# Performance work log

Hardware: AMD Instinct MI355X
Metric: run time of the kernel (lower is better)

Reference implementation:

```python
import jax, jax.numpy as jnp
import numpy as np

N = 50000       # nodes
E = 800000      # edges
F_IN = 197      # node_feature_dim
H = 256         # hidden_dim
HEADS = 8
HD = H // HEADS # 32
L = 5           # num_layers
FF = 4 * H      # 1024
C = 2           # num_classes
ED = 2          # edge_feature_dim
SCALE = float(np.sqrt(HD))


def _ln(x, g, b):
    m = x.mean(-1, keepdims=True)
    v = ((x - m) ** 2).mean(-1, keepdims=True)
    return (x - m) / jnp.sqrt(v + 1e-5) * g + b


def setup_inputs() -> dict:
    key = jax.random.key(0)
    ks = iter(jax.random.split(key, 40))
    d = {}
    d["x"] = jax.random.normal(next(ks), (N, F_IN), dtype=jnp.float32)
    d["edge_index"] = jax.random.randint(next(ks), (2, E), 0, N, dtype=jnp.int64)
    d["edge_attr"] = jax.random.normal(next(ks), (E, ED), dtype=jnp.float32)
    xav = lambda k, sh: jax.random.normal(k, sh, dtype=jnp.float32) * float(np.sqrt(2.0 / (sh[-2] + sh[-1])))
    # input projection + LN
    d["in_W"] = xav(next(ks), (F_IN, H)); d["in_b"] = jnp.zeros((H,), jnp.float32)
    d["in_g"] = jnp.ones((H,), jnp.float32); d["in_bb"] = jnp.zeros((H,), jnp.float32)
    # stacked per-layer params (leading dim L)
    d["Wq"] = xav(next(ks), (L, H, H)); d["Wk"] = xav(next(ks), (L, H, H)); d["Wv"] = xav(next(ks), (L, H, H))
    d["We"] = xav(next(ks), (L, ED, HEADS)); d["be"] = jnp.zeros((L, HEADS), jnp.float32)
    d["Wo"] = xav(next(ks), (L, H, H)); d["bo"] = jnp.zeros((L, H), jnp.float32)
    d["ln1_g"] = jnp.ones((L, H), jnp.float32); d["ln1_b"] = jnp.zeros((L, H), jnp.float32)
    d["ln2_g"] = jnp.ones((L, H), jnp.float32); d["ln2_b"] = jnp.zeros((L, H), jnp.float32)
    d["f1_W"] = xav(next(ks), (L, H, FF)); d["f1_b"] = jnp.zeros((L, FF), jnp.float32)
    d["f2_W"] = xav(next(ks), (L, FF, H)); d["f2_b"] = jnp.zeros((L, H), jnp.float32)
    # classifier
    d["cls1_W"] = xav(next(ks), (H, H // 2)); d["cls1_b"] = jnp.zeros((H // 2,), jnp.float32)
    d["cls2_W"] = xav(next(ks), (H // 2, C)); d["cls2_b"] = jnp.zeros((C,), jnp.float32)
    return d


def _forward(x, edge_index, edge_attr, in_W, in_b, in_g, in_bb,
             Wq, Wk, Wv, We, be, Wo, bo, ln1_g, ln1_b, ln2_g, ln2_b,
             f1_W, f1_b, f2_W, f2_b, cls1_W, cls1_b, cls2_W, cls2_b):
    src, dst = edge_index[0], edge_index[1]  # message flows src -> dst
    h = jax.nn.gelu(_ln(x @ in_W + in_b, in_g, in_bb), approximate=False)

    def layer(h, p):
        wq, wk, wv, we, b_e, wo, b_o, g1, b1, g2, b2, w1, bf1, w2, bf2 = p
        hn = _ln(h, g1, b1)
        q = (hn @ wq).reshape(-1, HEADS, HD)
        k = (hn @ wk).reshape(-1, HEADS, HD)
        v = (hn @ wv).reshape(-1, HEADS, HD)
        edge_bias = edge_attr @ we + b_e                        # (E, HEADS)
        score = (q[dst] * k[src]).sum(-1) / SCALE + edge_bias   # (E, HEADS)
        # segment softmax over destination nodes
        mx = jax.ops.segment_max(score, dst, num_segments=N)
        mx = jnp.where(jnp.isfinite(mx), mx, 0.0)
        ex = jnp.exp(score - mx[dst])
        denom = jax.ops.segment_sum(ex, dst, num_segments=N)
        w = ex / (denom[dst] + 1e-16)                           # (E, HEADS)
        msg = w[:, :, None] * v[src]                            # (E, HEADS, HD)
        agg = jax.ops.segment_sum(msg.reshape(-1, H), dst, num_segments=N)
        out = agg @ wo + b_o
        out = _ln(out + h, g2, b2)                              # residual_proj = Identity
        ffn = jax.nn.gelu(out @ w1 + bf1, approximate=False) @ w2 + bf2
        return out + ffn, None

    params = (Wq, Wk, Wv, We, be, Wo, bo, ln1_g, ln1_b, ln2_g, ln2_b, f1_W, f1_b, f2_W, f2_b)
    h, _ = jax.lax.scan(layer, h, params)
    logits = jax.nn.gelu(h @ cls1_W + cls1_b, approximate=False) @ cls2_W + cls2_b
    probs = jax.nn.softmax(logits, axis=-1)
    return logits, probs


def reference(x, edge_index, edge_attr, in_W, in_b, in_g, in_bb,
              Wq, Wk, Wv, We, be, Wo, bo, ln1_g, ln1_b, ln2_g, ln2_b,
              f1_W, f1_b, f2_W, f2_b, cls1_W, cls1_b, cls2_W, cls2_b):
    return _forward(x, edge_index, edge_attr, in_W, in_b, in_g, in_bb,
                    Wq, Wk, Wv, We, be, Wo, bo, ln1_g, ln1_b, ln2_g, ln2_b,
                    f1_W, f1_b, f2_W, f2_b, cls1_W, cls1_b, cls2_W, cls2_b)
```

## Files before the change

### kernel.cpp

```cpp
#include <hip/hip_runtime.h>
#include <math.h>

#define NN 50000
#define NE 800000
#define FIN 197
#define KIN 224
#define H 256
#define HEADS 8
#define HD 32
#define LAYERS 5
#define FF 1024
#define INV_SCALE 0.17677669529663687f

typedef __attribute__((ext_vector_type(8))) short short8;
typedef __attribute__((ext_vector_type(4))) float f32x4;
typedef unsigned short ushort;

__device__ __forceinline__ float gelu_f(float x) {
    float x2 = x * x;
    float u = __builtin_fmaf(0.044715f * x2, x, x);
    float e = __builtin_amdgcn_exp2f(-2.3022075f * u);
    return x * __builtin_amdgcn_rcpf(1.0f + e);
}
__device__ __forceinline__ ushort f2b(float f) {
    unsigned u = __float_as_uint(f);
    u += 0x7fffu + ((u >> 16) & 1u);
    return (ushort)(u >> 16);
}
__device__ __forceinline__ float b2f(ushort b) {
    return __uint_as_float(((unsigned)b) << 16);
}
__device__ __forceinline__ float dot2b(unsigned a, unsigned b) {
    float a0 = __uint_as_float(a << 16), a1 = __uint_as_float(a & 0xffff0000u);
    float b0 = __uint_as_float(b << 16), b1 = __uint_as_float(b & 0xffff0000u);
    return a0 * b0 + a1 * b1;
}

__device__ __forceinline__ void load16_lds(const ushort* gp, ushort* lp) {
    __builtin_amdgcn_global_load_lds(
        (const __attribute__((address_space(1))) unsigned int*)gp,
        (__attribute__((address_space(3))) unsigned int*)lp,
        16, 0, 0);
}

__global__ __launch_bounds__(256) void gemm_bf16_kernel(
    const ushort* __restrict__ A, int lda,
    const ushort* __restrict__ Bt,
    const float* __restrict__ bias,
    const float* __restrict__ res, int ldr,
    float* __restrict__ Cf, ushort* __restrict__ Cb, int ldc,
    int n, int K, int act, int gx)
{
    __shared__ ushort As[2][128 * 32];
    __shared__ ushort Bs[2][64 * 32];
    int tid = threadIdx.x;
    int lane = tid & 63;
    int wave = tid >> 6;

    int tiles_y = (n + 127) >> 7;
    int lin = blockIdx.x;
    int gsz = gx * 8;
    int group = lin / gsz;
    int rem = lin - group * gsz;
    int rows_left = tiles_y - group * 8;
    int rg = rows_left < 8 ? rows_left : 8;
    int r = rem % rg;
    int c = rem / rg;
    int brow = (group * 8 + r) * 128;
    int bcol = c * 64;

    f32x4 acc[2][4] = {};
    int m0 = lane & 15;
    int rdc = ((lane >> 4) ^ ((lane >> 1) & 3)) * 8;

    int rA = lane >> 2;
    int c8s = (((lane & 3) ^ ((lane >> 3) & 3)) * 8);

    long arow0, arow1, brow0;
    {
        int gr0 = brow + wave * 32 + rA;        if (gr0 >= n) gr0 = n - 1;
        int gr1 = brow + wave * 32 + 16 + rA;   if (gr1 >= n) gr1 = n - 1;
        arow0 = (long)gr0 * lda;
        arow1 = (long)gr1 * lda;
        brow0 = (long)(bcol + wave * 16 + rA) * K;
    }
    int loA0 = (wave * 32) * 32;
    int loA1 = (wave * 32 + 16) * 32;
    int loB  = (wave * 16) * 32;

    int nt = K >> 5;
    load16_lds(A + arow0 + c8s, &As[0][loA0]);
    load16_lds(A + arow1 + c8s, &As[0][loA1]);
    load16_lds(Bt + brow0 + c8s, &Bs[0][loB]);
    __syncthreads();

    for (int t = 0; t < nt; ++t) {
        int p = t & 1;
        if (t + 1 < nt) {
            int k0 = (t + 1) << 5;
            load16_lds(A + arow0 + k0 + c8s, &As[p ^ 1][loA0]);
            load16_lds(A + arow1 + k0 + c8s, &As[p ^ 1][loA1]);
            load16_lds(Bt + brow0 + k0 + c8s, &Bs[p ^ 1][loB]);
        }
        short8 af[2], bfr[4];
        #pragma unroll
        for (int i = 0; i < 2; ++i)
            af[i] = *(const short8*)&As[p][(wave * 32 + i * 16 + m0) * 32 + rdc];
        #pragma unroll
        for (int j = 0; j < 4; ++j)
            bfr[j] = *(const short8*)&Bs[p][(j * 16 + m0) * 32 + rdc];
        #pragma unroll
        for (int i = 0; i < 2; ++i)
            #pragma unroll
            for (int j = 0; j < 4; ++j)
                acc[i][j] = __builtin_amdgcn_mfma_f32_16x16x32_bf16(af[i], bfr[j], acc[i][j], 0, 0, 0);
        __syncthreads();
    }

    int crow0 = (lane >> 4) * 4;
    int ccol = lane & 15;
    #pragma unroll
    for (int i = 0; i < 2; ++i) {
        #pragma unroll
        for (int rr = 0; rr < 4; ++rr) {
            int grow = brow + wave * 32 + i * 16 + crow0 + rr;
            if (grow >= n) continue;
            #pragma unroll
            for (int j = 0; j < 4; ++j) {
                int gcol = bcol + j * 16 + ccol;
                float v = acc[i][j][rr];
                if (bias) v += bias[gcol];
                if (act) v = gelu_f(v);
                if (res) v += res[(long)grow * ldr + gcol];
                if (Cf) Cf[(long)grow * ldc + gcol] = v;
                if (Cb) Cb[(long)grow * ldc + gcol] = f2b(v);
            }
        }
    }
}

__global__ __launch_bounds__(256) void ln256_kernel(
    const float* __restrict__ af, const ushort* __restrict__ ab,
    const float* __restrict__ res,
    const float* __restrict__ g, const float* __restrict__ bta,
    float* __restrict__ outf, ushort* __restrict__ outb, int n, int post_gelu)
{
    int row = blockIdx.x * 4 + (threadIdx.x >> 6);
    if (row >= n) return;
    int lane = threadIdx.x & 63;
    float4 v;
    if (af) {
        v = *(const float4*)(af + (long)row * H + lane * 4);
    } else {
        ushort4 vb = *(const ushort4*)(ab + (long)row * H + lane * 4);
        v.x = b2f(vb.x); v.y = b2f(vb.y); v.z = b2f(vb.z); v.w = b2f(vb.w);
    }
    if (res) {
        float4 r = *(const float4*)(res + (long)row * H + lane * 4);
        v.x += r.x; v.y += r.y; v.z += r.z; v.w += r.w;
    }
    float s = v.x + v.y + v.z + v.w;
    #pragma unroll
    for (int off = 1; off < 64; off <<= 1) s += __shfl_xor(s, off);
    float mean = s * (1.0f / H);
    float dx = v.x - mean, dy = v.y - mean, dz = v.z - mean, dw = v.w - mean;
    float qs = dx * dx + dy * dy + dz * dz + dw * dw;
    #pragma unroll
    for (int off = 1; off < 64; off <<= 1) qs += __shfl_xor(qs, off);
    float rstd = rsqrtf(qs * (1.0f / H) + 1e-5f);
    float4 gg = *(const float4*)(g + lane * 4);
    float4 bb = *(const float4*)(bta + lane * 4);
    float4 o;
    o.x = dx * rstd * gg.x + bb.x;
    o.y = dy * rstd * gg.y + bb.y;
    o.z = dz * rstd * gg.z + bb.z;
    o.w = dw * rstd * gg.w + bb.w;
    if (post_gelu) { o.x = gelu_f(o.x); o.y = gelu_f(o.y); o.z = gelu_f(o.z); o.w = gelu_f(o.w); }
    if (outf) *(float4*)(outf + (long)row * H + lane * 4) = o;
    if (outb) {
        ushort4 ob = { f2b(o.x), f2b(o.y), f2b(o.z), f2b(o.w) };
        *(ushort4*)(outb + (long)row * H + lane * 4) = ob;
    }
}

__global__ __launch_bounds__(256) void xcast_kernel(const float* __restrict__ x,
                                                    ushort* __restrict__ xb)
{
    long i = (long)blockIdx.x * 256 + threadIdx.x;
    if (i >= (long)NN * KIN) return;
    int n = (int)(i / KIN), c = (int)(i % KIN);
    xb[i] = (c < FIN) ? f2b(x[(long)n * FIN + c]) : (ushort)0;
}

__global__ __launch_bounds__(256) void wtin_kernel(const float* __restrict__ W,
                                                   ushort* __restrict__ Wt)
{
    int i = blockIdx.x * 256 + threadIdx.x;
    if (i >= 256 * KIN) return;
    int m = i / KIN, k = i % KIN;
    Wt[i] = (k < FIN) ? f2b(W[(long)k * H + m]) : (ushort)0;
}

__global__ __launch_bounds__(256) void wtqkv_kernel(
    const float* __restrict__ Wq, const float* __restrict__ Wk,
    const float* __restrict__ Wv, ushort* __restrict__ out)
{
    long i = (long)blockIdx.x * 256 + threadIdx.x;
    if (i >= (long)LAYERS * 768 * 256) return;
    int l = (int)(i / (768 * 256));
    int r = (int)(i % (768 * 256));
    int m = r >> 8, k = r & 255;
    const float* W = (m < 256) ? Wq : ((m < 512) ? Wk : Wv);
    out[i] = f2b(W[(long)l * 65536 + (long)k * 256 + (m & 255)]);
}

__global__ __launch_bounds__(256) void wtgen_kernel(
    const float* __restrict__ W, ushort* __restrict__ out, int L, int K, int M)
{
    long i = (long)blockIdx.x * 256 + threadIdx.x;
    if (i >= (long)L * K * M) return;
    int l = (int)(i / ((long)K * M));
    int r = (int)(i % ((long)K * M));
    int m = r / K, k = r % K;
    out[i] = f2b(W[(long)l * K * M + (long)k * M + m]);
}

__global__ __launch_bounds__(256) void deg_kernel(const int* __restrict__ dst,
                                                   int* __restrict__ deg)
{
    int e = blockIdx.x * 256 + threadIdx.x;
    if (e >= NE) return;
    atomicAdd(&deg[dst[e]], 1);
}

__global__ __launch_bounds__(256) void scan1_kernel(const int* __restrict__ deg,
                                                     int* __restrict__ rowptr,
                                                     int* __restrict__ bsum)
{
    __shared__ int buf[256];
    int tid = threadIdx.x;
    int i = blockIdx.x * 256 + tid;
    int v = (i < NN) ? deg[i] : 0;
    buf[tid] = v;
    __syncthreads();
    #pragma unroll
    for (int off = 1; off < 256; off <<= 1) {
        int t = (tid >= off) ? buf[tid - off] : 0;
        __syncthreads();
        buf[tid] += t;
        __syncthreads();
    }
    if (i < NN) rowptr[i] = buf[tid] - v;
    if (tid == 255) bsum[blockIdx.x] = buf[255];
}

__global__ __launch_bounds__(256) void scan2_kernel(int* __restrict__ bsum, int nb)
{
    __shared__ int buf[256];
    int tid = threadIdx.x;
    int v = (tid < nb) ? bsum[tid] : 0;
    buf[tid] = v;
    __syncthreads();
    #pragma unroll
    for (int off = 1; off < 256; off <<= 1) {
        int t = (tid >= off) ? buf[tid - off] : 0;
        __syncthreads();
        buf[tid] += t;
        __syncthreads();
    }
    if (tid < nb) bsum[tid] = buf[tid] - v;
}

__global__ __launch_bounds__(256) void scan3_kernel(int* __restrict__ rowptr,
                                                     const int* __restrict__ bsum)
{
    int i = blockIdx.x * 256 + threadIdx.x;
    if (i < NN) rowptr[i] += bsum[blockIdx.x];
    if (i == 0) rowptr[NN] = NE;
}

__global__ __launch_bounds__(256) void fill_kernel(
    const int* __restrict__ src, const int* __restrict__ dst,
    const float* __restrict__ ea, const int* __restrict__ rowptr,
    int* __restrict__ cursor, int* __restrict__ csr_src,
    float2* __restrict__ csr_ea)
{
    int e = blockIdx.x * 256 + threadIdx.x;
    if (e >= NE) return;
    int d = dst[e];
    int pos = atomicAdd(&cursor[d], 1);
    int j = rowptr[d] + pos;
    csr_src[j] = src[e];
    csr_ea[j] = *(const float2*)(ea + 2 * e);
}

__global__ __launch_bounds__(256) void attn_kernel(
    const ushort* __restrict__ qkv,
    const int* __restrict__ rowptr, const int* __restrict__ csr_src,
    const float2* __restrict__ csr_ea,
    const float* __restrict__ We, const float* __restrict__ be,
    ushort* __restrict__ aggb)
{
    int node = blockIdx.x * 4 + (threadIdx.x >> 6);
    if (node >= NN) return;
    int lane = threadIdx.x & 63;
    int h = lane >> 3;
    const float L2E = 1.4426950408889634f;
    float w0 = We[h] * L2E, w1 = We[8 + h] * L2E, bb = be[h] * L2E;
    const float c1 = INV_SCALE * L2E;

    uint2 q2 = *(const uint2*)(qkv + (long)node * 768 + lane * 4);
    int jbeg = rowptr[node], jend = rowptr[node + 1];

    float m = -1e30f, l = 0.f;
    float a0 = 0.f, a1 = 0.f, a2 = 0.f, a3 = 0.f;

    uint2 kA = {0, 0}, vA = {0, 0}, kB = {0, 0}, vB = {0, 0};
    float2 eaA = {0.f, 0.f}, eaB = {0.f, 0.f};

    if (jbeg < jend) {
        int s = csr_src[jbeg]; eaA = csr_ea[jbeg];
        const ushort* kr = qkv + (long)s * 768 + 256;
        kA = *(const uint2*)(kr + lane * 4);
        vA = *(const uint2*)(kr + 256 + lane * 4);
    }
    if (jbeg + 1 < jend) {
        int s = csr_src[jbeg + 1]; eaB = csr_ea[jbeg + 1];
        const ushort* kr = qkv + (long)s * 768 + 256;
        kB = *(const uint2*)(kr + lane * 4);
        vB = *(const uint2*)(kr + 256 + lane * 4);
    }

    int j = jbeg;
    for (; j + 1 < jend; j += 2) {
        uint2 k1 = kA, v1 = vA, k2 = kB, v2 = vB;
        float2 e1 = eaA, e2 = eaB;
        if (j + 2 < jend) {
            int s = csr_src[j + 2]; eaA = csr_ea[j + 2];
            const ushort* kr = qkv + (long)s * 768 + 256;
            kA = *(const uint2*)(kr + lane * 4);
            vA = *(const uint2*)(kr + 256 + lane * 4);
        }
        if (j + 3 < jend) {
            int s = csr_src[j + 3]; eaB = csr_ea[j + 3];
            const ushort* kr = qkv + (long)s * 768 + 256;
            kB = *(const uint2*)(kr + lane * 4);
            vB = *(const uint2*)(kr + 256 + lane * 4);
        }
        float p1 = dot2b(q2.x, k1.x) + dot2b(q2.y, k1.y);
        float p2 = dot2b(q2.x, k2.x) + dot2b(q2.y, k2.y);
        p1 += __shfl_xor(p1, 1);  p2 += __shfl_xor(p2, 1);
        p1 += __shfl_xor(p1, 2);  p2 += __shfl_xor(p2, 2);
        p1 += __shfl_xor(p1, 4);  p2 += __shfl_xor(p2, 4);
        float s1 = p1 * c1 + e1.x * w0 + e1.y * w1 + bb;
        float s2 = p2 * c1 + e2.x * w0 + e2.y * w1 + bb;
        float mp = fmaxf(s1, s2);
        float x1 = __builtin_amdgcn_exp2f(s1 - mp);
        float x2 = __builtin_amdgcn_exp2f(s2 - mp);
        float lp = x1 + x2;
        float b0 = x1 * __uint_as_float(v1.x << 16)          + x2 * __uint_as_float(v2.x << 16);
        float b1 = x1 * __uint_as_float(v1.x & 0xffff0000u)  + x2 * __uint_as_float(v2.x & 0xffff0000u);
        float b2 = x1 * __uint_as_float(v1.y << 16)          + x2 * __uint_as_float(v2.y << 16);
        float b3 = x1 * __uint_as_float(v1.y & 0xffff0000u)  + x2 * __uint_as_float(v2.y & 0xffff0000u);
        float mn = fmaxf(m, mp);
        float so = __builtin_amdgcn_exp2f(m - mn);
        float sp = __builtin_amdgcn_exp2f(mp - mn);
        l  = l  * so + lp * sp;
        a0 = a0 * so + b0 * sp;
        a1 = a1 * so + b1 * sp;
        a2 = a2 * so + b2 * sp;
        a3 = a3 * so + b3 * sp;
        m = mn;
    }
    if (j < jend) {
        float p1 = dot2b(q2.x, kA.x) + dot2b(q2.y, kA.y);
        p1 += __shfl_xor(p1, 1);
        p1 += __shfl_xor(p1, 2);
        p1 += __shfl_xor(p1, 4);
        float s1 = p1 * c1 + eaA.x * w0 + eaA.y * w1 + bb;
        float mn = fmaxf(m, s1);
        float so = __builtin_amdgcn_exp2f(m - mn);
        float e  = __builtin_amdgcn_exp2f(s1 - mn);
        l  = l  * so + e;
        a0 = a0 * so + e * __uint_as_float(vA.x << 16);
        a1 = a1 * so + e * __uint_as_float(vA.x & 0xffff0000u);
        a2 = a2 * so + e * __uint_as_float(vA.y << 16);
        a3 = a3 * so + e * __uint_as_float(vA.y & 0xffff0000u);
    }
    float inv = 1.0f / (l + 1e-16f);
    ushort4 o = { f2b(a0 * inv), f2b(a1 * inv), f2b(a2 * inv), f2b(a3 * inv) };
    *(ushort4*)(aggb + (long)node * 256 + lane * 4) = o;
}

__global__ __launch_bounds__(256) void cls_kernel(
    const float* __restrict__ t1, const float* __restrict__ W,
    const float* __restrict__ b, float* __restrict__ out)
{
    int i = blockIdx.x * 256 + threadIdx.x;
    if (i >= NN) return;
    const float* tp = t1 + (long)i * 128;
    float a0 = 0.f, a1 = 0.f;
    #pragma unroll
    for (int j = 0; j < 128; j += 4) {
        float4 t = *(const float4*)(tp + j);
        a0 += t.x * W[(j + 0) * 2] + t.y * W[(j + 1) * 2] + t.z * W[(j + 2) * 2] + t.w * W[(j + 3) * 2];
        a1 += t.x * W[(j + 0) * 2 + 1] + t.y * W[(j + 1) * 2 + 1] + t.z * W[(j + 2) * 2 + 1] + t.w * W[(j + 3) * 2 + 1];
    }
    float l0 = a0 + b[0], l1 = a1 + b[1];
    out[(long)i * 2 + 0] = l0;
    out[(long)i * 2 + 1] = l1;
    float mx = fmaxf(l0, l1);
    float p0 = expf(l0 - mx), p1 = expf(l1 - mx);
    float sden = p0 + p1;
    out[2L * NN + (long)i * 2 + 0] = p0 / sden;
    out[2L * NN + (long)i * 2 + 1] = p1 / sden;
}

extern "C" void kernel_launch(void* const* d_in, const int* in_sizes, int n_in,
                              void* d_out, int out_size, void* d_ws, size_t ws_size,
                              hipStream_t stream) {
    const float* x      = (const float*)d_in[0];
    const int*   ei     = (const int*)d_in[1];
    const float* ea     = (const float*)d_in[2];
    const float* in_W   = (const float*)d_in[3];
    const float* in_b   = (const float*)d_in[4];
    const float* in_g   = (const float*)d_in[5];
    const float* in_bb  = (const float*)d_in[6];
    const float* Wq     = (const float*)d_in[7];
    const float* Wk     = (const float*)d_in[8];
    const float* Wv     = (const float*)d_in[9];
    const float* We     = (const float*)d_in[10];
    const float* be     = (const float*)d_in[11];
    const float* Wo     = (const float*)d_in[12];
    const float* bo     = (const float*)d_in[13];
    const float* ln1_g  = (const float*)d_in[14];
    const float* ln1_b  = (const float*)d_in[15];
    const float* ln2_g  = (const float*)d_in[16];
    const float* ln2_b  = (const float*)d_in[17];
    const float* f1_W   = (const float*)d_in[18];
    const float* f1_b   = (const float*)d_in[19];
    const float* f2_W   = (const float*)d_in[20];
    const float* f2_b   = (const float*)d_in[21];
    const float* cls1_W = (const float*)d_in[22];
    const float* cls1_b = (const float*)d_in[23];
    const float* cls2_W = (const float*)d_in[24];
    const float* cls2_b = (const float*)d_in[25];
    float* out = (float*)d_out;

    const int* src = ei;
    const int* dst = ei + NE;

    char* w = (char*)d_ws;
    float* B0 = (float*)w;            w += (size_t)NN * H * 4;
    ushort* hb = (ushort*)w;          w += (size_t)NN * H * 2;
    char* pool = w;                   w += (size_t)NN * 1024 * 2;
    ushort* qkv  = (ushort*)pool;
    ushort* aggb = (ushort*)(pool + (size_t)NN * 768 * 2);
    float*  tproj = (float*)pool;
    ushort* xb   = (ushort*)(pool + (size_t)NN * H * 4);
    ushort* tb   = (ushort*)pool;
    float*  t1   = (float*)pool;
    int* deg    = (int*)w;            w += (size_t)NN * 4;
    int* cursor = (int*)w;            w += (size_t)NN * 4;
    int* rowptr = (int*)w;            w += (size_t)(NN + 2) * 4;
    int* bsum   = (int*)w;            w += 1024;
    int* csr_src = (int*)w;           w += (size_t)NE * 4;
    float2* csr_ea = (float2*)w;      w += (size_t)NE * 8;
    ushort* wqkv_t = (ushort*)w;      w += (size_t)LAYERS * 768 * 256 * 2;
    ushort* wo_t  = (ushort*)w;       w += (size_t)LAYERS * 65536 * 2;
    ushort* f1_t  = (ushort*)w;       w += (size_t)LAYERS * 262144 * 2;
    ushort* f2_t  = (ushort*)w;       w += (size_t)LAYERS * 262144 * 2;
    ushort* c1_t  = (ushort*)w;       w += (size_t)32768 * 2;
    ushort* inw_t = (ushort*)w;       w += (size_t)256 * KIN * 2;

    dim3 blk(256);
    const int ln_grid = (NN + 3) / 4;
    const int e_grid = (NE + 255) / 256;
    const int n_grid = (NN + 255) / 256;
    const int ty = (NN + 127) / 128;

    hipMemsetAsync(deg, 0, (size_t)NN * 4, stream);
    hipMemsetAsync(cursor, 0, (size_t)NN * 4, stream);
    deg_kernel<<<e_grid, blk, 0, stream>>>(dst, deg);
    scan1_kernel<<<n_grid, blk, 0, stream>>>(deg, rowptr, bsum);
    scan2_kernel<<<1, blk, 0, stream>>>(bsum, n_grid);
    scan3_kernel<<<n_grid, blk, 0, stream>>>(rowptr, bsum);
    fill_kernel<<<e_grid, blk, 0, stream>>>(src, dst, ea, rowptr, cursor, csr_src, csr_ea);

    wtqkv_kernel<<<(int)(((long)LAYERS * 768 * 256 + 255) / 256), blk, 0, stream>>>(Wq, Wk, Wv, wqkv_t);
    wtgen_kernel<<<(int)(((long)LAYERS * 65536 + 255) / 256), blk, 0, stream>>>(Wo, wo_t, LAYERS, 256, 256);
    wtgen_kernel<<<(int)(((long)LAYERS * 262144 + 255) / 256), blk, 0, stream>>>(f1_W, f1_t, LAYERS, 256, 1024);
    wtgen_kernel<<<(int)(((long)LAYERS * 262144 + 255) / 256), blk, 0, stream>>>(f2_W, f2_t, LAYERS, 1024, 256);
    wtgen_kernel<<<(32768 + 255) / 256, blk, 0, stream>>>(cls1_W, c1_t, 1, 256, 128);
    wtin_kernel<<<(256 * KIN + 255) / 256, blk, 0, stream>>>(in_W, inw_t);

    xcast_kernel<<<(int)(((long)NN * KIN + 255) / 256), blk, 0, stream>>>(x, xb);
    {
        gemm_bf16_kernel<<<4 * ty, blk, 0, stream>>>(xb, KIN, inw_t, in_b, nullptr, 0,
                                                     tproj, nullptr, H, NN, KIN, 0, 4);
        ln256_kernel<<<ln_grid, blk, 0, stream>>>(tproj, nullptr, nullptr, in_g, in_bb, B0, nullptr, NN, 1);
    }

    for (int l = 0; l < LAYERS; ++l) {
        const float* we  = We + (long)l * 16;
        const float* bel = be + (long)l * 8;
        const float* bol = bo + (long)l * H;
        const float* g1 = ln1_g + (long)l * H;
        const float* b1 = ln1_b + (long)l * H;
        const float* g2 = ln2_g + (long)l * H;
        const float* b2 = ln2_b + (long)l * H;
        const float* bf1 = f1_b + (long)l * FF;
        const float* bf2 = f2_b + (long)l * H;

        ln256_kernel<<<ln_grid, blk, 0, stream>>>(B0, nullptr, nullptr, g1, b1, nullptr, hb, NN, 0);

        gemm_bf16_kernel<<<12 * ty, blk, 0, stream>>>(hb, H, wqkv_t + (long)l * 768 * 256,
            nullptr, nullptr, 0, nullptr, qkv, 768, NN, H, 0, 12);
        attn_kernel<<<(NN + 3) / 4, blk, 0, stream>>>(qkv, rowptr, csr_src, csr_ea, we, bel, aggb);

        gemm_bf16_kernel<<<4 * ty, blk, 0, stream>>>(aggb, H, wo_t + (long)l * 65536,
            bol, nullptr, 0, nullptr, qkv, H, NN, H, 0, 4);
        ln256_kernel<<<ln_grid, blk, 0, stream>>>(nullptr, qkv, B0, g2, b2, B0, hb, NN, 0);

        gemm_bf16_kernel<<<16 * ty, blk, 0, stream>>>(hb, H, f1_t + (long)l * 262144,
            bf1, nullptr, 0, nullptr, tb, FF, NN, H, 1, 16);
        gemm_bf16_kernel<<<4 * ty, blk, 0, stream>>>(tb, FF, f2_t + (long)l * 262144,
            bf2, B0, H, B0, (l == LAYERS - 1) ? hb : nullptr, H, NN, FF, 0, 4);
    }

    {
        gemm_bf16_kernel<<<2 * ty, blk, 0, stream>>>(hb, H, c1_t, cls1_b, nullptr, 0,
                                                     t1, nullptr, 128, NN, H, 1, 2);
        cls_kernel<<<n_grid, blk, 0, stream>>>(t1, cls2_W, cls2_b, out);
    }
}
```

Before: 2.385 ms.

## Sort attention nodes by degree and deepen edge prefetch to four

Adds a counting sort of nodes by in-degree (histogram, bin scan, scatter) so the attention kernel processes high-degree nodes first and places nodes of similar degree in the same block. This targets load imbalance and tail effects from variable-degree rows. The attention loop now keeps four edges of K/V in flight instead of two, to hide more gather latency, at the cost of more registers. Node order loses locality in the query and output writes.

```diff
diff --git a/kernel.cpp b/kernel.cpp
--- a/kernel.cpp
+++ b/kernel.cpp
@@ -294,15 +294,105 @@
     csr_ea[j] = *(const float2*)(ea + 2 * e);
 }
 
+__global__ __launch_bounds__(256) void hist_kernel(const int* __restrict__ rowptr,
+                                                   int* __restrict__ bins)
+{
+    int i = blockIdx.x * 256 + threadIdx.x;
+    if (i >= NN) return;
+    int d = rowptr[i + 1] - rowptr[i];
+    int b = d > 255 ? 0 : 255 - d;
+    atomicAdd(&bins[b], 1);
+}
+
+__global__ __launch_bounds__(256) void binscan_kernel(const int* __restrict__ bins,
+                                                      int* __restrict__ binoff)
+{
+    __shared__ int buf[256];
+    int tid = threadIdx.x;
+    int v = bins[tid];
+    buf[tid] = v;
+    __syncthreads();
+    #pragma unroll
+    for (int off = 1; off < 256; off <<= 1) {
+        int t = (tid >= off) ? buf[tid - off] : 0;
+        __syncthreads();
+        buf[tid] += t;
+        __syncthreads();
+    }
+    binoff[tid] = buf[tid] - v;
+}
+
+__global__ __launch_bounds__(256) void order_kernel(const int* __restrict__ rowptr,
+                                                    int* __restrict__ binoff,
+                                                    int* __restrict__ order)
+{
+    int i = blockIdx.x * 256 + threadIdx.x;
+    if (i >= NN) return;
+    int d = rowptr[i + 1] - rowptr[i];
+    int b = d > 255 ? 0 : 255 - d;
+    int pos = atomicAdd(&binoff[b], 1);
+    order[pos] = i;
+}
+
+#define LOADE(idx, kbuf, vbuf, ebuf)                                   \
+    { int s_ = csr_src[idx]; ebuf = csr_ea[idx];                       \
+      const ushort* kr_ = qkv + (long)s_ * 768 + 256;                  \
+      kbuf = *(const uint2*)(kr_ + lane * 4);                          \
+      vbuf = *(const uint2*)(kr_ + 256 + lane * 4); }
+
+#define PAIR(k1, v1, e1, k2, v2, e2)                                               \
+    { float p1 = dot2b(q2.x, (k1).x) + dot2b(q2.y, (k1).y);                        \
+      float p2 = dot2b(q2.x, (k2).x) + dot2b(q2.y, (k2).y);                        \
+      p1 += __shfl_xor(p1, 1);  p2 += __shfl_xor(p2, 1);                           \
+      p1 += __shfl_xor(p1, 2);  p2 += __shfl_xor(p2, 2);                           \
+      p1 += __shfl_xor(p1, 4);  p2 += __shfl_xor(p2, 4);                           \
+      float s1 = p1 * c1 + (e1).x * w0 + (e1).y * w1 + bb;                         \
+      float s2 = p2 * c1 + (e2).x * w0 + (e2).y * w1 + bb;                         \
+      float mp = fmaxf(s1, s2);                                                    \
+      float x1 = __builtin_amdgcn_exp2f(s1 - mp);                                  \
+      float x2 = __builtin_amdgcn_exp2f(s2 - mp);                                  \
+      float lp = x1 + x2;                                                          \
+      float b0 = x1 * __uint_as_float((v1).x << 16)         + x2 * __uint_as_float((v2).x << 16);          \
+      float b1 = x1 * __uint_as_float((v1).x & 0xffff0000u) + x2 * __uint_as_float((v2).x & 0xffff0000u);  \
+      float b2 = x1 * __uint_as_float((v1).y << 16)         + x2 * __uint_as_float((v2).y << 16);          \
+      float b3 = x1 * __uint_as_float((v1).y & 0xffff0000u) + x2 * __uint_as_float((v2).y & 0xffff0000u);  \
+      float mn = fmaxf(m, mp);                                                     \
+      float so = __builtin_amdgcn_exp2f(m - mn);                                   \
+      float sp = __builtin_amdgcn_exp2f(mp - mn);                                  \
+      l  = l  * so + lp * sp;                                                      \
+      a0 = a0 * so + b0 * sp;                                                      \
+      a1 = a1 * so + b1 * sp;                                                      \
+      a2 = a2 * so + b2 * sp;                                                      \
+      a3 = a3 * so + b3 * sp;                                                      \
+      m = mn; }
+
+#define SINGLE(kb, vb, eb)                                                         \
+    { float p1 = dot2b(q2.x, (kb).x) + dot2b(q2.y, (kb).y);                        \
+      p1 += __shfl_xor(p1, 1);                                                     \
+      p1 += __shfl_xor(p1, 2);                                                     \
+      p1 += __shfl_xor(p1, 4);                                                     \
+      float s1 = p1 * c1 + (eb).x * w0 + (eb).y * w1 + bb;                         \
+      float mn = fmaxf(m, s1);                                                     \
+      float so = __builtin_amdgcn_exp2f(m - mn);                                   \
+      float e_ = __builtin_amdgcn_exp2f(s1 - mn);                                  \
+      l  = l  * so + e_;                                                           \
+      a0 = a0 * so + e_ * __uint_as_float((vb).x << 16);                           \
+      a1 = a1 * so + e_ * __uint_as_float((vb).x & 0xffff0000u);                   \
+      a2 = a2 * so + e_ * __uint_as_float((vb).y << 16);                           \
+      a3 = a3 * so + e_ * __uint_as_float((vb).y & 0xffff0000u);                   \
+      m = mn; }
+
 __global__ __launch_bounds__(256) void attn_kernel(
     const ushort* __restrict__ qkv,
     const int* __restrict__ rowptr, const int* __restrict__ csr_src,
     const float2* __restrict__ csr_ea,
     const float* __restrict__ We, const float* __restrict__ be,
+    const int* __restrict__ order,
     ushort* __restrict__ aggb)
 {
-    int node = blockIdx.x * 4 + (threadIdx.x >> 6);
-    if (node >= NN) return;
+    int widx = blockIdx.x * 4 + (threadIdx.x >> 6);
+    if (widx >= NN) return;
+    int node = order[widx];
     int lane = threadIdx.x & 63;
     int h = lane >> 3;
     const float L2E = 1.4426950408889634f;
@@ -315,78 +405,29 @@
     float m = -1e30f, l = 0.f;
     float a0 = 0.f, a1 = 0.f, a2 = 0.f, a3 = 0.f;
 
-    uint2 kA = {0, 0}, vA = {0, 0}, kB = {0, 0}, vB = {0, 0};
-    float2 eaA = {0.f, 0.f}, eaB = {0.f, 0.f};
-
-    if (jbeg < jend) {
-        int s = csr_src[jbeg]; eaA = csr_ea[jbeg];
-        const ushort* kr = qkv + (long)s * 768 + 256;
-        kA = *(const uint2*)(kr + lane * 4);
-        vA = *(const uint2*)(kr + 256 + lane * 4);
-    }
-    if (jbeg + 1 < jend) {
-        int s = csr_src[jbeg + 1]; eaB = csr_ea[jbeg + 1];
-        const ushort* kr = qkv + (long)s * 768 + 256;
-        kB = *(const uint2*)(kr + lane * 4);
-        vB = *(const uint2*)(kr + 256 + lane * 4);
-    }
+    uint2 k0v = {0,0}, v0v = {0,0}, k1v = {0,0}, v1v = {0,0};
+    uint2 k2v = {0,0}, v2v = {0,0}, k3v = {0,0}, v3v = {0,0};
+    float2 e0v = {0.f,0.f}, e1v = {0.f,0.f}, e2v = {0.f,0.f}, e3v = {0.f,0.f};
+
+    if (jbeg + 0 < jend) LOADE(jbeg + 0, k0v, v0v, e0v);
+    if (jbeg + 1 < jend) LOADE(jbeg + 1, k1v, v1v, e1v);
+    if (jbeg + 2 < jend) LOADE(jbeg + 2, k2v, v2v, e2v);
+    if (jbeg + 3 < jend) LOADE(jbeg + 3, k3v, v3v, e3v);
 
     int j = jbeg;
-    for (; j + 1 < jend; j += 2) {
-        uint2 k1 = kA, v1 = vA, k2 = kB, v2 = vB;
-        float2 e1 = eaA, e2 = eaB;
-        if (j + 2 < jend) {
-            int s = csr_src[j + 2]; eaA = csr_ea[j + 2];
-            const ushort* kr = qkv + (long)s * 768 + 256;
-            kA = *(const uint2*)(kr + lane * 4);
-            vA = *(const uint2*)(kr + 256 + lane * 4);
-        }
-        if (j + 3 < jend) {
-            int s = csr_src[j + 3]; eaB = csr_ea[j + 3];
-            const ushort* kr = qkv + (long)s * 768 + 256;
-            kB = *(const uint2*)(kr + lane * 4);
-            vB = *(const uint2*)(kr + 256 + lane * 4);
-        }
-        float p1 = dot2b(q2.x, k1.x) + dot2b(q2.y, k1.y);
-        float p2 = dot2b(q2.x, k2.x) + dot2b(q2.y, k2.y);
-        p1 += __shfl_xor(p1, 1);  p2 += __shfl_xor(p2, 1);
-        p1 += __shfl_xor(p1, 2);  p2 += __shfl_xor(p2, 2);
-        p1 += __shfl_xor(p1, 4);  p2 += __shfl_xor(p2, 4);
-        float s1 = p1 * c1 + e1.x * w0 + e1.y * w1 + bb;
-        float s2 = p2 * c1 + e2.x * w0 + e2.y * w1 + bb;
-        float mp = fmaxf(s1, s2);
-        float x1 = __builtin_amdgcn_exp2f(s1 - mp);
-        float x2 = __builtin_amdgcn_exp2f(s2 - mp);
-        float lp = x1 + x2;
-        float b0 = x1 * __uint_as_float(v1.x << 16)          + x2 * __uint_as_float(v2.x << 16);
-        float b1 = x1 * __uint_as_float(v1.x & 0xffff0000u)  + x2 * __uint_as_float(v2.x & 0xffff0000u);
-        float b2 = x1 * __uint_as_float(v1.y << 16)          + x2 * __uint_as_float(v2.y << 16);
-        float b3 = x1 * __uint_as_float(v1.y & 0xffff0000u)  + x2 * __uint_as_float(v2.y & 0xffff0000u);
-        float mn = fmaxf(m, mp);
-        float so = __builtin_amdgcn_exp2f(m - mn);
-        float sp = __builtin_amdgcn_exp2f(mp - mn);
-        l  = l  * so + lp * sp;
-        a0 = a0 * so + b0 * sp;
-        a1 = a1 * so + b1 * sp;
-        a2 = a2 * so + b2 * sp;
-        a3 = a3 * so + b3 * sp;
-        m = mn;
-    }
-    if (j < jend) {
-        float p1 = dot2b(q2.x, kA.x) + dot2b(q2.y, kA.y);
-        p1 += __shfl_xor(p1, 1);
-        p1 += __shfl_xor(p1, 2);
-        p1 += __shfl_xor(p1, 4);
-        float s1 = p1 * c1 + eaA.x * w0 + eaA.y * w1 + bb;
-        float mn = fmaxf(m, s1);
-        float so = __builtin_amdgcn_exp2f(m - mn);
-        float e  = __builtin_amdgcn_exp2f(s1 - mn);
-        l  = l  * so + e;
-        a0 = a0 * so + e * __uint_as_float(vA.x << 16);
-        a1 = a1 * so + e * __uint_as_float(vA.x & 0xffff0000u);
-        a2 = a2 * so + e * __uint_as_float(vA.y << 16);
-        a3 = a3 * so + e * __uint_as_float(vA.y & 0xffff0000u);
-    }
+    for (; j + 3 < jend; j += 4) {
+        PAIR(k0v, v0v, e0v, k1v, v1v, e1v);
+        if (j + 4 < jend) LOADE(j + 4, k0v, v0v, e0v);
+        if (j + 5 < jend) LOADE(j + 5, k1v, v1v, e1v);
+        PAIR(k2v, v2v, e2v, k3v, v3v, e3v);
+        if (j + 6 < jend) LOADE(j + 6, k2v, v2v, e2v);
+        if (j + 7 < jend) LOADE(j + 7, k3v, v3v, e3v);
+    }
+    int rleft = jend - j;
+    if (rleft >= 2) PAIR(k0v, v0v, e0v, k1v, v1v, e1v);
+    if (rleft == 3) SINGLE(k2v, v2v, e2v);
+    if (rleft == 1) SINGLE(k0v, v0v, e0v);
+
     float inv = 1.0f / (l + 1e-16f);
     ushort4 o = { f2b(a0 * inv), f2b(a1 * inv), f2b(a2 * inv), f2b(a3 * inv) };
     *(ushort4*)(aggb + (long)node * 256 + lane * 4) = o;
@@ -472,6 +513,9 @@
     ushort* f2_t  = (ushort*)w;       w += (size_t)LAYERS * 262144 * 2;
     ushort* c1_t  = (ushort*)w;       w += (size_t)32768 * 2;
     ushort* inw_t = (ushort*)w;       w += (size_t)256 * KIN * 2;
+    int* bins   = (int*)w;            w += 1024;
+    int* binoff = (int*)w;            w += 1024;
+    int* order  = (int*)w;            w += (size_t)NN * 4;
 
     dim3 blk(256);
     const int ln_grid = (NN + 3) / 4;
@@ -481,11 +525,16 @@
 
     hipMemsetAsync(deg, 0, (size_t)NN * 4, stream);
     hipMemsetAsync(cursor, 0, (size_t)NN * 4, stream);
+    hipMemsetAsync(bins, 0, 1024, stream);
     deg_kernel<<<e_grid, blk, 0, stream>>>(dst, deg);
     scan1_kernel<<<n_grid, blk, 0, stream>>>(deg, rowptr, bsum);
     scan2_kernel<<<1, blk, 0, stream>>>(bsum, n_grid);
     scan3_kernel<<<n_grid, blk, 0, stream>>>(rowptr, bsum);
     fill_kernel<<<e_grid, blk, 0, stream>>>(src, dst, ea, rowptr, cursor, csr_src, csr_ea);
+
+    hist_kernel<<<n_grid, blk, 0, stream>>>(rowptr, bins);
+    binscan_kernel<<<1, blk, 0, stream>>>(bins, binoff);
+    order_kernel<<<n_grid, blk, 0, stream>>>(rowptr, binoff, order);
 
     wtqkv_kernel<<<(int)(((long)LAYERS * 768 * 256 + 255) / 256), blk, 0, stream>>>(Wq, Wk, Wv, wqkv_t);
     wtgen_kernel<<<(int)(((long)LAYERS * 65536 + 255) / 256), blk, 0, stream>>>(Wo, wo_t, LAYERS, 256, 256);
@@ -516,7 +565,7 @@
 
         gemm_bf16_kernel<<<12 * ty, blk, 0, stream>>>(hb, H, wqkv_t + (long)l * 768 * 256,
             nullptr, nullptr, 0, nullptr, qkv, 768, NN, H, 0, 12);
-        attn_kernel<<<(NN + 3) / 4, blk, 0, stream>>>(qkv, rowptr, csr_src, csr_ea, we, bel, aggb);
+        attn_kernel<<<(NN + 3) / 4, blk, 0, stream>>>(qkv, rowptr, csr_src, csr_ea, we, bel, order, aggb);
 
         gemm_bf16_kernel<<<4 * ty, blk, 0, stream>>>(aggb, H, wo_t + (long)l * 65536,
             bol, nullptr, 0, nullptr, qkv, H, NN, H, 0, 4);
```

After: 2.636 ms. 10.5% more time.
